# Performance work log

Hardware: AMD Instinct MI355X
Metric: run time of the kernel (lower is better)

Reference implementation:

```python
import jax, jax.numpy as jnp
import numpy as np

N = 65536      # samples
DX = 1024      # X features
DY = 1024      # Y features
D = 256        # projected width (x_net/y_net output)
LAMX = 0.1
LAMY = 0.1
SIGMA = 0.5    # STG gate noise std (eval-mode deterministic gate)
EPS = 0.001    # regularizer used in original code


def setup_inputs() -> dict:
    key = jax.random.key(0)
    ks = jax.random.split(key, 8)
    X = jax.random.normal(ks[0], (N, DX), dtype=jnp.float32)
    Y = jax.random.normal(ks[1], (N, DY), dtype=jnp.float32)
    # StochasticGates params (mu per input feature)
    mu_x = 0.01 * jax.random.normal(ks[2], (DX,), dtype=jnp.float32)
    mu_y = 0.01 * jax.random.normal(ks[3], (DY,), dtype=jnp.float32)
    # per-view linear nets (x_net: DX->D, y_net: DY->D)
    Wx = jax.random.normal(ks[4], (DX, D), dtype=jnp.float32) / np.sqrt(DX)
    bx = jnp.zeros((D,), dtype=jnp.float32)
    Wy = jax.random.normal(ks[5], (DY, D), dtype=jnp.float32) / np.sqrt(DY)
    by = jnp.zeros((D,), dtype=jnp.float32)
    return {"X": X, "Y": Y, "mu_x": mu_x, "mu_y": mu_y,
            "Wx": Wx, "bx": bx, "Wy": Wy, "by": by}


def _stg_gate(mu):
    # deterministic (eval) hard gate: clamp(mu + 0.5, 0, 1)
    return jnp.clip(mu + 0.5, 0.0, 1.0)


def _stg_reg(mu, lam):
    # lam * mean(P(gate > 0)) = lam * mean(Phi(mu/sigma))  [Gaussian CDF]
    return lam * jnp.mean(0.5 * (1.0 + jax.lax.erf(mu / (SIGMA * jnp.sqrt(2.0)))))


def _cov(a, b):
    # matches torch: (b.T @ a).T / (N-1) == a.T @ b / (N-1)
    n = a.shape[0]
    return (a.T @ b) / (n - 1)


def _inv_sqrt_sym(A):
    # A^(-1/2) via eigendecomposition; A symmetric so eigh == eig with V^-1 = V.T
    w, V = jnp.linalg.eigh(A)
    return (V * (w + EPS) ** (-0.5)) @ V.T


def _corr(Xh, Yh):
    d = Xh.shape[1]
    psi_x = Xh - Xh.mean(axis=0)
    psi_y = Yh - Yh.mean(axis=0)
    C_yy = _cov(psi_y, psi_y)
    C_yx = _cov(psi_y, psi_x)
    C_xy = _cov(psi_x, psi_y)
    C_xx = _cov(psi_x, psi_x)
    I = jnp.eye(d, dtype=Xh.dtype)
    C_yy_inv_root = _inv_sqrt_sym(C_yy + EPS * I)
    C_xx_inv = jnp.linalg.inv(C_xx + EPS * I)
    M = C_yy_inv_root @ C_yx @ C_xx_inv @ C_xy @ C_yy_inv_root
    return jnp.trace(M) / d


def reference(X, Y, mu_x, mu_y, Wx, bx, Wy, by):
    Xh = (X * _stg_gate(mu_x)) @ Wx + bx   # [N, D]
    Yh = (Y * _stg_gate(mu_y)) @ Wy + by   # [N, D]
    loss = -_corr(Xh, Yh) + _stg_reg(mu_x, LAMX) + _stg_reg(mu_y, LAMY)
    return loss
```

## Files before the change

kernel.cpp:

```cpp
#include <hip/hip_runtime.h>

#define N_S   65536
#define DXF   1024
#define DD    256
#define NM1   65535.0f
#define EPSR  0.001f

typedef __attribute__((ext_vector_type(4)))  float          f32x4;
typedef __attribute__((ext_vector_type(16))) float          f32x16;
typedef __attribute__((ext_vector_type(8)))  short          bf16x8;
typedef __attribute__((ext_vector_type(4)))  unsigned short ushort4_t;
typedef __attribute__((ext_vector_type(8)))  unsigned short ushort8_t;

__device__ __forceinline__ unsigned short f2bf(float f){
  unsigned u = __float_as_uint(f);
  u += 0x7fffu + ((u >> 16) & 1u);
  return (unsigned short)(u >> 16);
}
__device__ __forceinline__ float bf2f(unsigned short h){
  return __uint_as_float(((unsigned)h) << 16);
}
__device__ __forceinline__ f32x4 mfma16(bf16x8 a, bf16x8 b, f32x4 c){
  return __builtin_amdgcn_mfma_f32_16x16x32_bf16(a, b, c, 0, 0, 0);
}
__device__ __forceinline__ f32x16 mfma32(bf16x8 a, bf16x8 b, f32x16 c){
  return __builtin_amdgcn_mfma_f32_32x32x16_bf16(a, b, c, 0, 0, 0);
}
__device__ __forceinline__ void gld_lds16(const void* g, void* l){
  __builtin_amdgcn_global_load_lds(
      (const __attribute__((address_space(1))) unsigned int*)g,
      (__attribute__((address_space(3))) unsigned int*)l, 16, 0, 0);
}

__global__ void k_prep(const float* __restrict__ Wx, const float* __restrict__ Wy,
                       const float* __restrict__ mux, const float* __restrict__ muy,
                       unsigned short* __restrict__ WTx, unsigned short* __restrict__ WTy,
                       float* __restrict__ scal){
  int v = blockIdx.y;
  const float* W  = v ? Wy  : Wx;
  const float* mu = v ? muy : mux;
  unsigned short* WT = v ? WTy : WTx;
  int j = threadIdx.x;
  if (j < 4){
    float ph = 0.5f * (1.f + erff(mu[blockIdx.x * 4 + j] * 1.41421356237f));
    atomicAdd(scal + 2 + v, 9.765625e-5f * ph);
  }
  #pragma unroll
  for (int r = 0; r < 4; ++r){
    int k = blockIdx.x * 4 + r;
    float g = fminf(fmaxf(mu[k] + 0.5f, 0.f), 1.f);
    WT[(size_t)(k >> 3) * 2048 + j * 8 + (k & 7)] = f2bf(g * W[(size_t)k * DD + j]);
  }
}

__global__ __launch_bounds__(512, 8) void k_gemm8(
    const float* __restrict__ X, const float* __restrict__ Y,
    const unsigned short* __restrict__ WTx, const unsigned short* __restrict__ WTy,
    unsigned short* __restrict__ Xhb, unsigned short* __restrict__ Yhb){
  const float* A = blockIdx.z ? Y : X;
  const unsigned short* WT = blockIdx.z ? WTy : WTx;
  unsigned short* Out = blockIdx.z ? Yhb : Xhb;

  __shared__ unsigned short As[64][40];
  __shared__ unsigned short Bs[2][4][256][8];

  int tid = threadIdx.x, lane = tid & 63, wid = tid >> 6;
  int wr = wid >> 2, wc = wid & 3;
  int row0 = blockIdx.x * 64;

  f32x4 acc[2][4] = {};

  int s_row = tid >> 3, s_kq = tid & 7;
  const float* ap = A + (size_t)(row0 + s_row) * DXF + s_kq * 4;

  auto stageB = [&](int buf, int ks){
    #pragma unroll
    for (int i = 0; i < 2; ++i){
      int cg = (wid >> 2) * 2 + i;
      gld_lds16(WT + (size_t)(ks * 4 + (wid & 3)) * 2048 + (cg * 64 + lane) * 8,
                &Bs[buf][wid & 3][cg * 64][0]);
    }
  };
  auto storeAs = [&](float4 a){
    union { unsigned u[2]; ushort4_t v; } r;
    asm("v_cvt_pk_bf16_f32 %0, %1, %2" : "=v"(r.u[0]) : "v"(a.x), "v"(a.y));
    asm("v_cvt_pk_bf16_f32 %0, %1, %2" : "=v"(r.u[1]) : "v"(a.z), "v"(a.w));
    *(ushort4_t*)&As[s_row][s_kq * 4] = r.v;
  };

  float4 a0, ar;
  stageB(0, 0);
  asm volatile("" ::: "memory");
  a0 = *(const float4*)(ap);
  asm volatile("" ::: "memory");
  stageB(1, 1);
  asm volatile("s_waitcnt vmcnt(2)" ::: "memory");
  storeAs(a0);
  ar = *(const float4*)(ap + 32);
  asm volatile("s_waitcnt lgkmcnt(0)" ::: "memory");
  __builtin_amdgcn_s_barrier();

  for (int ks = 0; ks < 32; ++ks){
    int buf = ks & 1;
    bf16x8 af0 = *(const bf16x8*)&As[wr * 32 + (lane & 15)][(lane >> 4) * 8];
    bf16x8 af1 = *(const bf16x8*)&As[wr * 32 + 16 + (lane & 15)][(lane >> 4) * 8];
    #pragma unroll
    for (int ni = 0; ni < 4; ++ni){
      bf16x8 bf = *(const bf16x8*)&Bs[buf][lane >> 4][wc * 64 + ni * 16 + (lane & 15)][0];
      acc[0][ni] = mfma16(af0, bf, acc[0][ni]);
      acc[1][ni] = mfma16(af1, bf, acc[1][ni]);
    }
    if (ks == 31) break;
    __builtin_amdgcn_s_barrier();
    if (ks + 2 < 32){
      stageB(buf, ks + 2);
      asm volatile("s_waitcnt vmcnt(2)" ::: "memory");
    } else {
      asm volatile("s_waitcnt vmcnt(0)" ::: "memory");
    }
    storeAs(ar);
    if (ks + 2 < 32){
      asm volatile("" ::: "memory");
      ar = *(const float4*)(ap + (ks + 2) * 32);
    }
    asm volatile("s_waitcnt lgkmcnt(0)" ::: "memory");
    __builtin_amdgcn_s_barrier();
  }

  __syncthreads();
  unsigned short* tl = &Bs[0][0][0][0];
  #pragma unroll
  for (int mi = 0; mi < 2; ++mi)
    #pragma unroll
    for (int ni = 0; ni < 4; ++ni)
      #pragma unroll
      for (int rr = 0; rr < 4; ++rr){
        int r = wr * 32 + mi * 16 + (lane >> 4) * 4 + rr;
        int c = wc * 64 + ni * 16 + (lane & 15);
        tl[r * 256 + c] = f2bf(acc[mi][ni][rr]);
      }
  __syncthreads();
  unsigned short* ob = Out + (size_t)row0 * DD;
  #pragma unroll
  for (int r = 0; r < 4; ++r){
    int off = r * 4096 + tid * 8;
    *(ushort8_t*)(ob + off) = *(const ushort8_t*)(tl + off);
  }
}

__global__ __launch_bounds__(512) void k_gram(
    const unsigned short* __restrict__ Xhb, const unsigned short* __restrict__ Yhb,
    float* __restrict__ part, float* __restrict__ sx, float* __restrict__ sy, int P){
  int type = blockIdx.z;
  int p = blockIdx.x;
  int chunk = N_S / P;
  int r0 = p * chunk;
  const unsigned short* Asrc = (type == 0) ? Xhb : Yhb;
  const unsigned short* Bsrc = (type == 1) ? Yhb : Xhb;
  bool dualB = (type == 2);

  __shared__ unsigned short At[256][40];
  __shared__ unsigned short Bt[256][40];

  int tid = threadIdx.x;
  int lane = tid & 63, wid = tid >> 6;
  int wr = wid >> 1, wc = wid & 1;

  f32x4 acc[4][8] = {};
  float cs0 = 0.f, cs1 = 0.f;

  int cp  = tid & 127;
  int kb0 = tid >> 7;

  unsigned ua[2][4], ub[2][4];

  auto loadT = [&](int ks){
    int base = r0 + ks * 32;
    #pragma unroll
    for (int r = 0; r < 2; ++r){
      int kb = kb0 + r * 4;
      #pragma unroll
      for (int kr = 0; kr < 4; ++kr){
        ua[r][kr] = *(const unsigned*)(Asrc + (size_t)(base + kb * 4 + kr) * DD + cp * 2);
        if (dualB)
          ub[r][kr] = *(const unsigned*)(Bsrc + (size_t)(base + kb * 4 + kr) * DD + cp * 2);
      }
    }
  };
  auto storeT = [&](){
    #pragma unroll
    for (int r = 0; r < 2; ++r){
      int kb = kb0 + r * 4;
      ushort4_t lo = { (unsigned short)ua[r][0], (unsigned short)ua[r][1],
                       (unsigned short)ua[r][2], (unsigned short)ua[r][3] };
      ushort4_t hi = { (unsigned short)(ua[r][0] >> 16), (unsigned short)(ua[r][1] >> 16),
                       (unsigned short)(ua[r][2] >> 16), (unsigned short)(ua[r][3] >> 16) };
      *(ushort4_t*)&At[cp * 2][kb * 4]     = lo;
      *(ushort4_t*)&At[cp * 2 + 1][kb * 4] = hi;
      if (type < 2){
        #pragma unroll
        for (int kr = 0; kr < 4; ++kr){
          cs0 += bf2f((unsigned short)ua[r][kr]);
          cs1 += bf2f((unsigned short)(ua[r][kr] >> 16));
        }
      }
      if (dualB){
        ushort4_t lob = { (unsigned short)ub[r][0], (unsigned short)ub[r][1],
                          (unsigned short)ub[r][2], (unsigned short)ub[r][3] };
        ushort4_t hib = { (unsigned short)(ub[r][0] >> 16), (unsigned short)(ub[r][1] >> 16),
                          (unsigned short)(ub[r][2] >> 16), (unsigned short)(ub[r][3] >> 16) };
        *(ushort4_t*)&Bt[cp * 2][kb * 4]     = lob;
        *(ushort4_t*)&Bt[cp * 2 + 1][kb * 4] = hib;
      }
    }
  };

  unsigned short (*Btp)[40] = dualB ? Bt : At;

  int KS = chunk / 32;
  loadT(0);
  for (int ks = 0; ks < KS; ++ks){
    __syncthreads();
    storeT();
    __syncthreads();
    if (ks + 1 < KS) loadT(ks + 1);
    bf16x8 af[4], bfv[8];
    #pragma unroll
    for (int mi = 0; mi < 4; ++mi)
      af[mi] = *(const bf16x8*)&At[wr * 64 + mi * 16 + (lane & 15)][(lane >> 4) * 8];
    #pragma unroll
    for (int ni = 0; ni < 8; ++ni)
      bfv[ni] = *(const bf16x8*)&Btp[wc * 128 + ni * 16 + (lane & 15)][(lane >> 4) * 8];
    #pragma unroll
    for (int mi = 0; mi < 4; ++mi)
      #pragma unroll
      for (int ni = 0; ni < 8; ++ni)
        acc[mi][ni] = mfma16(af[mi], bfv[ni], acc[mi][ni]);
  }

  float* dst = part + ((size_t)p * 3 + type) * 65536;
  #pragma unroll
  for (int mi = 0; mi < 4; ++mi)
    #pragma unroll
    for (int ni = 0; ni < 8; ++ni)
      #pragma unroll
      for (int rr = 0; rr < 4; ++rr){
        int grow = wr * 64 + mi * 16 + (lane >> 4) * 4 + rr;
        int gcol = wc * 128 + ni * 16 + (lane & 15);
        dst[(size_t)grow * 256 + gcol] = acc[mi][ni][rr];
      }

  if (type < 2){
    __syncthreads();
    float* red = (float*)&At[0][0];
    red[kb0 * 256 + cp * 2]     = cs0;
    red[kb0 * 256 + cp * 2 + 1] = cs1;
    __syncthreads();
    if (tid < 256){
      float s = red[tid] + red[256 + tid] + red[512 + tid] + red[768 + tid];
      atomicAdd((type == 0 ? sx : sy) + tid, s);
    }
  }
}

__global__ void k_reduce(const float* __restrict__ part, const float* __restrict__ sx,
                         const float* __restrict__ sy, float* __restrict__ Am,
                         float* __restrict__ Bm,
                         unsigned short* __restrict__ Abf, unsigned short* __restrict__ Bbf,
                         unsigned short* __restrict__ Cbf, unsigned short* __restrict__ CbfT,
                         float* __restrict__ scal, int P){
  __shared__ float r2[256];
  int i = blockIdx.x, j = threadIdx.x;
  size_t idx = (size_t)i * 256 + j;
  float gxx = 0.f, gyy = 0.f, gyx = 0.f;
  for (int p = 0; p < P; ++p){
    const float* b = part + (size_t)p * 3 * 65536;
    gxx += b[idx];
    gyy += b[65536 + idx];
    gyx += b[131072 + idx];
  }
  float invn1 = 1.f / NM1;
  float invn  = 1.f / (float)N_S;
  float sxi = sx[i], sxj = sx[j], syi = sy[i], syj = sy[j];
  float diag = (i == j) ? 1.f : 0.f;
  float am = (gyy - syi * syj * invn) * invn1 + diag * (2.f * EPSR);
  float bm = (gxx - sxi * sxj * invn) * invn1 + diag * EPSR;
  float cv = (gyx - syi * sxj * invn) * invn1;
  Am[idx] = am;  Bm[idx] = bm;
  Abf[idx] = f2bf(am);
  Bbf[idx] = f2bf(bm);
  Cbf[idx] = f2bf(cv);
  CbfT[(size_t)j * 256 + i] = f2bf(cv);
  r2[j] = fabsf(am);
  __syncthreads();
  for (int s = 128; s > 0; s >>= 1){ if (j < s) r2[j] += r2[j + s]; __syncthreads(); }
  if (j == 0) atomicMax((unsigned*)scal + 5, __float_as_uint(r2[0]));
  __syncthreads();
  r2[j] = fabsf(bm);
  __syncthreads();
  for (int s = 128; s > 0; s >>= 1){ if (j < s) r2[j] += r2[j + s]; __syncthreads(); }
  if (j == 0) atomicMax((unsigned*)scal + 6, __float_as_uint(r2[0]));
}

__global__ void k_x1(const float* __restrict__ Am, const float* __restrict__ Bm,
                     unsigned short* __restrict__ X0, const float* __restrict__ scal){
  int m = blockIdx.y;
  const unsigned* su = (const unsigned*)scal;
  float al = 1.9f / __uint_as_float(su[5 + m]);
  const float* M = m ? Bm : Am;
  int e = blockIdx.x * 512 + threadIdx.x;
  float v = -al * al * M[e];
  if ((e >> 8) == (e & 255)) v += 2.f * al;
  X0[m * 65536 + e] = f2bf(v);
}

__global__ __launch_bounds__(512) void k_it(
    const unsigned short* __restrict__ Abf, const unsigned short* __restrict__ Bbf,
    const unsigned short* __restrict__ Xc, unsigned short* __restrict__ Xn){
  int m = blockIdx.y, j = blockIdx.x;
  const unsigned short* M  = m ? Bbf : Abf;
  const unsigned short* Xm = Xc + m * 65536;
  unsigned short*       Xo = Xn + m * 65536;

  __shared__ unsigned short XJ[32 * 256];
  __shared__ unsigned short TT[32 * 256];

  int tid = threadIdx.x, lane = tid & 63, w = tid >> 6;
  int r31 = lane & 31, kh = lane >> 5;

  #pragma unroll
  for (int i = 0; i < 2; ++i){
    int rl = w * 4 + i * 2 + kh;
    int cg = ((lane & 31) - rl) & 31;
    gld_lds16(Xm + (size_t)(j * 32 + rl) * 256 + cg * 8, &XJ[(w * 4 + i * 2) * 256]);
  }
  asm volatile("s_waitcnt vmcnt(0)" ::: "memory");
  __builtin_amdgcn_s_barrier();

  f32x16 acc = {};
  const unsigned short* arow = M + (size_t)(w * 32 + r31) * 256 + kh * 8;
  #pragma unroll
  for (int ks = 0; ks < 16; ++ks){
    bf16x8 af = *(const bf16x8*)(arow + ks * 16);
    int ch = ((ks * 2 + kh) + r31) & 31;
    bf16x8 bf = *(const bf16x8*)&XJ[r31 * 256 + ch * 8];
    acc = mfma32(af, bf, acc);
  }
  #pragma unroll
  for (int reg = 0; reg < 16; ++reg){
    int kk = w * 32 + (reg & 3) + ((reg >> 2) << 3) + (kh << 2);
    int ch = ((kk >> 3) + r31) & 31;
    TT[r31 * 256 + ch * 8 + (kk & 7)] = f2bf(acc[reg]);
  }
  __syncthreads();

  f32x16 acc2 = {};
  const unsigned short* xrow = Xm + (size_t)(w * 32 + r31) * 256 + kh * 8;
  #pragma unroll
  for (int ks = 0; ks < 16; ++ks){
    bf16x8 af = *(const bf16x8*)(xrow + ks * 16);
    int ch = ((ks * 2 + kh) + r31) & 31;
    bf16x8 bf = *(const bf16x8*)&TT[r31 * 256 + ch * 8];
    acc2 = mfma32(af, bf, acc2);
  }
  #pragma unroll
  for (int reg = 0; reg < 16; ++reg){
    int row = w * 32 + (reg & 3) + ((reg >> 2) << 3) + (kh << 2);
    int ch = ((row >> 3) + r31) & 31;
    float xv = bf2f(XJ[r31 * 256 + ch * 8 + (row & 7)]);
    Xo[(size_t)row * 256 + j * 32 + r31] = f2bf(2.f * xv - acc2[reg]);
  }
}

__global__ __launch_bounds__(512) void k_uv(
    const unsigned short* __restrict__ Xf,
    const unsigned short* __restrict__ Cbf, const unsigned short* __restrict__ CbfT,
    float* __restrict__ U, float* __restrict__ W){
  int m = blockIdx.y, j = blockIdx.x;
  __shared__ unsigned short BJ[32 * 256];
  int tid = threadIdx.x, lane = tid & 63, w = tid >> 6;
  int r31 = lane & 31, kh = lane >> 5;
  const unsigned short* Brows = m ? (Xf + 65536) : CbfT;
  const unsigned short* Arows = m ? Cbf : Xf;
  float* D = m ? W : U;

  #pragma unroll
  for (int i = 0; i < 2; ++i){
    int rl = w * 4 + i * 2 + kh;
    int cg = ((lane & 31) - rl) & 31;
    gld_lds16(Brows + (size_t)(j * 32 + rl) * 256 + cg * 8, &BJ[(w * 4 + i * 2) * 256]);
  }
  asm volatile("s_waitcnt vmcnt(0)" ::: "memory");
  __builtin_amdgcn_s_barrier();

  f32x16 acc = {};
  const unsigned short* ar = Arows + (size_t)(w * 32 + r31) * 256 + kh * 8;
  #pragma unroll
  for (int ks = 0; ks < 16; ++ks){
    bf16x8 af = *(const bf16x8*)(ar + ks * 16);
    int ch = ((ks * 2 + kh) + r31) & 31;
    bf16x8 bf = *(const bf16x8*)&BJ[r31 * 256 + ch * 8];
    acc = mfma32(af, bf, acc);
  }
  #pragma unroll
  for (int reg = 0; reg < 16; ++reg){
    int row = w * 32 + (reg & 3) + ((reg >> 2) << 3) + (kh << 2);
    D[(size_t)row * 256 + j * 32 + r31] = acc[reg];
  }
}

__global__ __launch_bounds__(1024) void k_fin(const float* __restrict__ U,
                                              const float* __restrict__ W,
                                              const float* __restrict__ scal,
                                              float* __restrict__ out){
  __shared__ float red[1024];
  int tid = threadIdx.x;
  float t = 0.f;
  #pragma unroll
  for (int r = 0; r < 16; ++r){
    int i = r * 4096 + tid * 4;
    float4 u = *(const float4*)(U + i);
    float4 w = *(const float4*)(W + i);
    t += u.x * w.x + u.y * w.y + u.z * w.z + u.w * w.w;
  }
  red[tid] = t; __syncthreads();
  for (int s = 512; s > 0; s >>= 1){ if (tid < s) red[tid] += red[tid + s]; __syncthreads(); }
  if (tid == 0) out[0] = -red[0] / 256.f + scal[2] + scal[3];
}

extern "C" void kernel_launch(void* const* d_in, const int* in_sizes, int n_in,
                              void* d_out, int out_size, void* d_ws, size_t ws_size,
                              hipStream_t stream){
  (void)in_sizes; (void)n_in; (void)out_size;
  const float* X   = (const float*)d_in[0];
  const float* Y   = (const float*)d_in[1];
  const float* mux = (const float*)d_in[2];
  const float* muy = (const float*)d_in[3];
  const float* Wx  = (const float*)d_in[4];
  const float* Wy  = (const float*)d_in[6];
  float* out = (float*)d_out;
  char* ws = (char*)d_ws;

  const size_t MB = 1ull << 20;
  const size_t KB = 1024;
  size_t oXHB = 0;
  size_t oYHB = 32 * MB;
  size_t oWTX = 64 * MB;
  size_t oWTY = oWTX + 512 * KB;
  size_t oSX  = oWTY + 512 * KB;
  size_t oSY  = oSX + 4 * KB;
  size_t oSC  = oSY + 4 * KB;
  size_t oA   = oSC + 4 * KB;
  size_t oB   = oA   + 256 * KB;
  size_t oABF = oB   + 256 * KB;
  size_t oBBF = oABF + 128 * KB;
  size_t oCBF = oBBF + 128 * KB;
  size_t oCBT = oCBF + 128 * KB;
  size_t oX0  = oCBT + 128 * KB;
  size_t oX1  = oX0  + 256 * KB;
  size_t oTB  = oX1  + 256 * KB;
  size_t oU   = oTB  + 256 * KB;
  size_t oV   = oU   + 256 * KB;
  size_t oPart = 68 * MB;

  size_t per = 3ull * 65536 * 4;
  int P = 64;
  while (P > 8 && oPart + (size_t)P * per > ws_size) P >>= 1;

  unsigned short* Xhb = (unsigned short*)(ws + oXHB);
  unsigned short* Yhb = (unsigned short*)(ws + oYHB);
  unsigned short* WTx = (unsigned short*)(ws + oWTX);
  unsigned short* WTy = (unsigned short*)(ws + oWTY);
  float* sx   = (float*)(ws + oSX);
  float* sy   = (float*)(ws + oSY);
  float* scal = (float*)(ws + oSC);
  float* Am   = (float*)(ws + oA);
  float* Bm   = (float*)(ws + oB);
  unsigned short* Abf  = (unsigned short*)(ws + oABF);
  unsigned short* Bbf  = (unsigned short*)(ws + oBBF);
  unsigned short* Cbf  = (unsigned short*)(ws + oCBF);
  unsigned short* CbfT = (unsigned short*)(ws + oCBT);
  unsigned short* X0   = (unsigned short*)(ws + oX0);
  unsigned short* X1   = (unsigned short*)(ws + oX1);
  float* U    = (float*)(ws + oU);
  float* V    = (float*)(ws + oV);
  float* part = (float*)(ws + oPart);

  hipMemsetAsync(ws + oSX, 0, 12 * KB, stream);

  k_prep<<<dim3(256, 2), 256, 0, stream>>>(Wx, Wy, mux, muy, WTx, WTy, scal);
  k_gemm8<<<dim3(1024, 1, 2), 512, 0, stream>>>(X, Y, WTx, WTy, Xhb, Yhb);
  k_gram<<<dim3(P, 1, 3), 512, 0, stream>>>(Xhb, Yhb, part, sx, sy, P);
  k_reduce<<<256, 256, 0, stream>>>(part, sx, sy, Am, Bm, Abf, Bbf, Cbf, CbfT, scal, P);

  k_x1<<<dim3(128, 2), 512, 0, stream>>>(Am, Bm, X0, scal);
  k_it<<<dim3(8, 2), 512, 0, stream>>>(Abf, Bbf, X0, X1);
  k_it<<<dim3(8, 2), 512, 0, stream>>>(Abf, Bbf, X1, X0);
  k_it<<<dim3(8, 2), 512, 0, stream>>>(Abf, Bbf, X0, X1);
  k_it<<<dim3(8, 2), 512, 0, stream>>>(Abf, Bbf, X1, X0);
  k_it<<<dim3(8, 2), 512, 0, stream>>>(Abf, Bbf, X0, X1);
  k_uv<<<dim3(8, 2), 512, 0, stream>>>(X1, Cbf, CbfT, U, V);
  k_fin<<<1, 1024, 0, stream>>>(U, V, scal, out);
}
```

Before: 307.9 us.

## Restructure projection GEMM: load W fragments directly to registers, larger A k-chunks

Rewrites the X/Y projection GEMM so each wave loads its B (weight) fragments straight from global memory into registers instead of staging them through LDS. The A tile is now staged in k-chunks of 128 with double-buffered LDS, which cuts the number of barriers from 32 to 8. The warp layout changes so each wave covers all 64 rows and 32 columns, with explicit vmcnt waits interleaving loads and MFMAs. The trade-offs are higher register pressure (launch bounds lowered to 4 blocks per CU) and weight reads that now rely on the cache.

```diff
diff --git a/kernel.cpp b/kernel.cpp
--- a/kernel.cpp
+++ b/kernel.cpp
@@ -31,6 +31,8 @@
       (const __attribute__((address_space(1))) unsigned int*)g,
       (__attribute__((address_space(3))) unsigned int*)l, 16, 0, 0);
 }
+
+#define VMCNT(N) asm volatile("s_waitcnt vmcnt(" #N ")" ::: "memory")
 
 __global__ void k_prep(const float* __restrict__ Wx, const float* __restrict__ Wy,
                        const float* __restrict__ mux, const float* __restrict__ muy,
@@ -53,7 +55,7 @@
   }
 }
 
-__global__ __launch_bounds__(512, 8) void k_gemm8(
+__global__ __launch_bounds__(512, 4) void k_gemm9(
     const float* __restrict__ X, const float* __restrict__ Y,
     const unsigned short* __restrict__ WTx, const unsigned short* __restrict__ WTy,
     unsigned short* __restrict__ Xhb, unsigned short* __restrict__ Yhb){
@@ -61,83 +63,108 @@
   const unsigned short* WT = blockIdx.z ? WTy : WTx;
   unsigned short* Out = blockIdx.z ? Yhb : Xhb;
 
-  __shared__ unsigned short As[64][40];
-  __shared__ unsigned short Bs[2][4][256][8];
+  __shared__ unsigned short As[2][64][136];
 
   int tid = threadIdx.x, lane = tid & 63, wid = tid >> 6;
-  int wr = wid >> 2, wc = wid & 3;
   int row0 = blockIdx.x * 64;
 
-  f32x4 acc[2][4] = {};
-
-  int s_row = tid >> 3, s_kq = tid & 7;
-  const float* ap = A + (size_t)(row0 + s_row) * DXF + s_kq * 4;
-
-  auto stageB = [&](int buf, int ks){
-    #pragma unroll
-    for (int i = 0; i < 2; ++i){
-      int cg = (wid >> 2) * 2 + i;
-      gld_lds16(WT + (size_t)(ks * 4 + (wid & 3)) * 2048 + (cg * 64 + lane) * 8,
-                &Bs[buf][wid & 3][cg * 64][0]);
-    }
+  f32x4 acc[4][2] = {};
+
+  int s_row = tid >> 3, s_f4 = tid & 7;
+  const float* ap = A + (size_t)(row0 + s_row) * DXF + s_f4 * 4;
+
+  const unsigned short* bB = WT + (size_t)(lane >> 4) * 2048
+                           + (wid * 32 + (lane & 15)) * 8;
+
+  float4 ar0, ar1, ar2, ar3;
+  auto writeA = [&](int b){
+    union { unsigned u[2]; ushort4_t v; } w;
+    asm("v_cvt_pk_bf16_f32 %0, %1, %2" : "=v"(w.u[0]) : "v"(ar0.x), "v"(ar0.y));
+    asm("v_cvt_pk_bf16_f32 %0, %1, %2" : "=v"(w.u[1]) : "v"(ar0.z), "v"(ar0.w));
+    *(ushort4_t*)&As[b][s_row][s_f4 * 4] = w.v;
+    asm("v_cvt_pk_bf16_f32 %0, %1, %2" : "=v"(w.u[0]) : "v"(ar1.x), "v"(ar1.y));
+    asm("v_cvt_pk_bf16_f32 %0, %1, %2" : "=v"(w.u[1]) : "v"(ar1.z), "v"(ar1.w));
+    *(ushort4_t*)&As[b][s_row][s_f4 * 4 + 32] = w.v;
+    asm("v_cvt_pk_bf16_f32 %0, %1, %2" : "=v"(w.u[0]) : "v"(ar2.x), "v"(ar2.y));
+    asm("v_cvt_pk_bf16_f32 %0, %1, %2" : "=v"(w.u[1]) : "v"(ar2.z), "v"(ar2.w));
+    *(ushort4_t*)&As[b][s_row][s_f4 * 4 + 64] = w.v;
+    asm("v_cvt_pk_bf16_f32 %0, %1, %2" : "=v"(w.u[0]) : "v"(ar3.x), "v"(ar3.y));
+    asm("v_cvt_pk_bf16_f32 %0, %1, %2" : "=v"(w.u[1]) : "v"(ar3.z), "v"(ar3.w));
+    *(ushort4_t*)&As[b][s_row][s_f4 * 4 + 96] = w.v;
   };
-  auto storeAs = [&](float4 a){
-    union { unsigned u[2]; ushort4_t v; } r;
-    asm("v_cvt_pk_bf16_f32 %0, %1, %2" : "=v"(r.u[0]) : "v"(a.x), "v"(a.y));
-    asm("v_cvt_pk_bf16_f32 %0, %1, %2" : "=v"(r.u[1]) : "v"(a.z), "v"(a.w));
-    *(ushort4_t*)&As[s_row][s_kq * 4] = r.v;
+  auto loadA = [&](int kc){
+    const float* p = ap + kc * 128;
+    ar0 = *(const float4*)(p);
+    ar1 = *(const float4*)(p + 32);
+    ar2 = *(const float4*)(p + 64);
+    ar3 = *(const float4*)(p + 96);
   };
 
-  float4 a0, ar;
-  stageB(0, 0);
-  asm volatile("" ::: "memory");
-  a0 = *(const float4*)(ap);
-  asm volatile("" ::: "memory");
-  stageB(1, 1);
-  asm volatile("s_waitcnt vmcnt(2)" ::: "memory");
-  storeAs(a0);
-  ar = *(const float4*)(ap + 32);
+  loadA(0);
+  VMCNT(0);
+  writeA(0);
   asm volatile("s_waitcnt lgkmcnt(0)" ::: "memory");
   __builtin_amdgcn_s_barrier();
 
-  for (int ks = 0; ks < 32; ++ks){
-    int buf = ks & 1;
-    bf16x8 af0 = *(const bf16x8*)&As[wr * 32 + (lane & 15)][(lane >> 4) * 8];
-    bf16x8 af1 = *(const bf16x8*)&As[wr * 32 + 16 + (lane & 15)][(lane >> 4) * 8];
-    #pragma unroll
-    for (int ni = 0; ni < 4; ++ni){
-      bf16x8 bf = *(const bf16x8*)&Bs[buf][lane >> 4][wc * 64 + ni * 16 + (lane & 15)][0];
-      acc[0][ni] = mfma16(af0, bf, acc[0][ni]);
-      acc[1][ni] = mfma16(af1, bf, acc[1][ni]);
+#define GSTEP(S, BA, BB) { \
+    bf16x8 af0 = *(const bf16x8*)&As[buf][     (lane & 15)][S * 32 + (lane >> 4) * 8]; \
+    bf16x8 af1 = *(const bf16x8*)&As[buf][16 + (lane & 15)][S * 32 + (lane >> 4) * 8]; \
+    bf16x8 af2 = *(const bf16x8*)&As[buf][32 + (lane & 15)][S * 32 + (lane >> 4) * 8]; \
+    bf16x8 af3 = *(const bf16x8*)&As[buf][48 + (lane & 15)][S * 32 + (lane >> 4) * 8]; \
+    acc[0][0] = mfma16(af0, BA, acc[0][0]); acc[0][1] = mfma16(af0, BB, acc[0][1]); \
+    acc[1][0] = mfma16(af1, BA, acc[1][0]); acc[1][1] = mfma16(af1, BB, acc[1][1]); \
+    acc[2][0] = mfma16(af2, BA, acc[2][0]); acc[2][1] = mfma16(af2, BB, acc[2][1]); \
+    acc[3][0] = mfma16(af3, BA, acc[3][0]); acc[3][1] = mfma16(af3, BB, acc[3][1]); }
+
+  #pragma unroll
+  for (int c = 0; c < 8; ++c){
+    int buf = c & 1;
+    const unsigned short* bc = bB + c * 32768;
+    bf16x8 b0a = *(const bf16x8*)(bc);
+    bf16x8 b0b = *(const bf16x8*)(bc + 128);
+    bf16x8 b1a = *(const bf16x8*)(bc + 8192);
+    bf16x8 b1b = *(const bf16x8*)(bc + 8320);
+    bf16x8 b2a = *(const bf16x8*)(bc + 16384);
+    bf16x8 b2b = *(const bf16x8*)(bc + 16512);
+    bf16x8 b3a = *(const bf16x8*)(bc + 24576);
+    bf16x8 b3b = *(const bf16x8*)(bc + 24704);
+    asm volatile("" ::: "memory");
+    if (c < 7) loadA(c + 1);
+
+    if (c < 7) { VMCNT(10); } else { VMCNT(6); }
+    __builtin_amdgcn_sched_barrier(0);
+    GSTEP(0, b0a, b0b)
+    if (c < 7) { VMCNT(8); } else { VMCNT(4); }
+    __builtin_amdgcn_sched_barrier(0);
+    GSTEP(1, b1a, b1b)
+    if (c < 7) { VMCNT(6); } else { VMCNT(2); }
+    __builtin_amdgcn_sched_barrier(0);
+    GSTEP(2, b2a, b2b)
+    if (c < 7) { VMCNT(4); } else { VMCNT(0); }
+    __builtin_amdgcn_sched_barrier(0);
+    GSTEP(3, b3a, b3b)
+
+    if (c < 7){
+      VMCNT(0);
+      __builtin_amdgcn_sched_barrier(0);
+      writeA(buf ^ 1);
+      asm volatile("s_waitcnt lgkmcnt(0)" ::: "memory");
+      __builtin_amdgcn_s_barrier();
     }
-    if (ks == 31) break;
-    __builtin_amdgcn_s_barrier();
-    if (ks + 2 < 32){
-      stageB(buf, ks + 2);
-      asm volatile("s_waitcnt vmcnt(2)" ::: "memory");
-    } else {
-      asm volatile("s_waitcnt vmcnt(0)" ::: "memory");
-    }
-    storeAs(ar);
-    if (ks + 2 < 32){
-      asm volatile("" ::: "memory");
-      ar = *(const float4*)(ap + (ks + 2) * 32);
-    }
-    asm volatile("s_waitcnt lgkmcnt(0)" ::: "memory");
-    __builtin_amdgcn_s_barrier();
-  }
+  }
+#undef GSTEP
 
   __syncthreads();
-  unsigned short* tl = &Bs[0][0][0][0];
-  #pragma unroll
-  for (int mi = 0; mi < 2; ++mi)
-    #pragma unroll
-    for (int ni = 0; ni < 4; ++ni)
+  unsigned short* tl = &As[0][0][0];
+  #pragma unroll
+  for (int r = 0; r < 4; ++r)
+    #pragma unroll
+    for (int t = 0; t < 2; ++t)
       #pragma unroll
       for (int rr = 0; rr < 4; ++rr){
-        int r = wr * 32 + mi * 16 + (lane >> 4) * 4 + rr;
-        int c = wc * 64 + ni * 16 + (lane & 15);
-        tl[r * 256 + c] = f2bf(acc[mi][ni][rr]);
+        int row = r * 16 + (lane >> 4) * 4 + rr;
+        int col = wid * 32 + t * 16 + (lane & 15);
+        tl[row * 256 + col] = f2bf(acc[r][t][rr]);
       }
   __syncthreads();
   unsigned short* ob = Out + (size_t)row0 * DD;
@@ -489,7 +516,7 @@
   hipMemsetAsync(ws + oSX, 0, 12 * KB, stream);
 
   k_prep<<<dim3(256, 2), 256, 0, stream>>>(Wx, Wy, mux, muy, WTx, WTy, scal);
-  k_gemm8<<<dim3(1024, 1, 2), 512, 0, stream>>>(X, Y, WTx, WTy, Xhb, Yhb);
+  k_gemm9<<<dim3(1024, 1, 2), 512, 0, stream>>>(X, Y, WTx, WTy, Xhb, Yhb);
   k_gram<<<dim3(P, 1, 3), 512, 0, stream>>>(Xhb, Yhb, part, sx, sy, P);
   k_reduce<<<256, 256, 0, stream>>>(part, sx, sy, Am, Bm, Abf, Bbf, Cbf, CbfT, scal, P);
 
```

After: 286.1 us. 7.1% less time.
